# Kernel tuning notes

Measured on AMD Instinct MI355X. Metric: run time of the kernel, lower is better.

The kernel has to match this reference:

```python
import jax, jax.numpy as jnp
import numpy as np

B, N, D, H = 8, 1024, 1024, 16
P = D // H
FACTOR = 1.0 / np.sqrt(P)
DFF = 4 * D


def layernorm(x, g, b, eps=1e-5):
    mu = jnp.mean(x, axis=-1, keepdims=True)
    var = jnp.var(x, axis=-1, keepdims=True)
    return (x - mu) * jax.lax.rsqrt(var + eps) * g + b


def setup_inputs() -> dict:
    key = jax.random.key(0)
    ks = jax.random.split(key, 6)
    s = 0.02
    return {
        "x": jax.random.normal(ks[0], (B, N, D), jnp.float32),
        "prior_attn": jax.random.normal(ks[1], (B, N, N), jnp.float32),
        "Wqkv": jax.random.normal(ks[2], (D, 3 * D), jnp.float32) * s,
        "bqkv": jnp.zeros((3 * D,), jnp.float32),
        "alpha": jnp.asarray(1.0, jnp.float32),
        "ln1_g": jnp.ones((D,), jnp.float32),
        "ln1_b": jnp.zeros((D,), jnp.float32),
        "ln2_g": jnp.ones((D,), jnp.float32),
        "ln2_b": jnp.zeros((D,), jnp.float32),
        "w1": jax.random.normal(ks[3], (D, DFF), jnp.float32) * s,
        "b1": jnp.zeros((DFF,), jnp.float32),
        "w2": jax.random.normal(ks[4], (DFF, D), jnp.float32) * s,
        "b2": jnp.zeros((D,), jnp.float32),
    }


def reference(x, prior_attn, Wqkv, bqkv, alpha, ln1_g, ln1_b, ln2_g, ln2_b, w1, b1, w2, b2):
    b, n, d = x.shape
    # --- PriorMSA on ln_1(x) ---
    z1 = layernorm(x, ln1_g, ln1_b)
    qkv = z1 @ Wqkv + bqkv                      # [b, n, 3d]
    q, k, v = jnp.split(qkv, 3, axis=-1)
    q = q.reshape(b, n, H, P)
    k = k.reshape(b, n, H, P)
    v = v.reshape(b, n, H, P)
    raw = jnp.einsum('bihp,bjhp->bhij', q, k)   # [b, h, n, n]
    raw = raw + alpha * prior_attn[:, None, :, :]
    attn = jax.nn.softmax(raw * FACTOR, axis=-1)
    out = jnp.einsum('bhij,bjhp->bihp', attn, v).reshape(b, n, d)
    s1 = x + out                                 # residual (no out-projection in source)
    # --- MLP on ln_2(s1) ---
    z2 = layernorm(s1, ln2_g, ln2_b)
    mlp = jax.nn.gelu(z2 @ w1 + b1) @ w2 + b2
    return s1 + mlp
```

## Files before the change

kernel.cpp:

```cpp
#include <hip/hip_runtime.h>
#include <hip/hip_bf16.h>
#include <stdint.h>


typedef __attribute__((ext_vector_type(8))) short short8;
typedef __attribute__((ext_vector_type(4))) float f32x4;

__device__ __forceinline__ int is_bf16_in(const void* ln1g) {
  return *(const uint32_t*)ln1g == 0x3F803F80u;
}
__device__ __forceinline__ float bf2f(uint16_t u) {
  union { uint32_t i; float f; } v; v.i = ((uint32_t)u) << 16; return v.f;
}
__device__ __forceinline__ uint16_t f2bf(float f) {
  union { float f; uint32_t i; } v; v.f = f;
  uint32_t r = v.i + 0x7FFFu + ((v.i >> 16) & 1u);
  return (uint16_t)(r >> 16);
}
__device__ __forceinline__ float ldin(const void* p, size_t i, int bf) {
  return bf ? bf2f(((const uint16_t*)p)[i]) : ((const float*)p)[i];
}
__device__ __forceinline__ uint32_t pack_bf(float a, float b) {
  union { float f; uint32_t u; } ua, ub; ua.f = a; ub.f = b;
  return ((ua.u + 0x8000u) >> 16) | ((ub.u + 0x8000u) & 0xFFFF0000u);
}

typedef __attribute__((address_space(1))) void gvoid;
typedef __attribute__((address_space(3))) void lvoid;
__device__ __forceinline__ void gld16(const uint16_t* g, uint16_t* l) {
  __builtin_amdgcn_global_load_lds((const gvoid*)g, (lvoid*)l, 16, 0, 0);
}

__device__ __forceinline__ float gelu_f(float x) {
  float t1 = x * x;
  float s = fmaf(t1, -0.1029498f, -2.3023457f);
  float e = __builtin_amdgcn_exp2f(x * s);
  return x * __builtin_amdgcn_rcpf(1.0f + e);
}

template<int EPI>
__global__ __launch_bounds__(256) void gemm_bt(
    const uint16_t* __restrict__ A, const uint16_t* __restrict__ Bt,
    const void* __restrict__ bias, const void* __restrict__ flagsrc,
    void* __restrict__ Cout, const float* __restrict__ resid,
    int M, int N, int K)
{
  __shared__ __align__(16) uint16_t As[8192];
  __shared__ __align__(16) uint16_t Bs[8192];
  const int t = threadIdx.x;
  const int wv = t >> 6;
  const int lane = t & 63;
  const int ln = lane & 15, quad = lane >> 4;
  const int wm = (wv & 1) * 64, wn = (wv >> 1) * 64;
  const int row0 = blockIdx.y * 128, col0 = blockIdx.x * 128;

  auto mk = [&](const uint16_t* Pb, int base, int c) -> const uint16_t* {
    int m = c >> 3, s = c & 7;
    int kc = s ^ (m & 7);
    return Pb + (size_t)(base + m) * K + kc * 8;
  };
  const uint16_t* ap[4];
  const uint16_t* bp[4];
  uint16_t* lA[4];
  uint16_t* lB[4];
#pragma unroll
  for (int q = 0; q < 4; ++q) {
    ap[q] = mk(A, row0, t + q * 256);
    bp[q] = mk(Bt, col0, t + q * 256);
    lA[q] = &As[(q * 256 + wv * 64) * 8];
    lB[q] = &Bs[(q * 256 + wv * 64) * 8];
  }

  int aidx[2][4], bidx[2][4];
#pragma unroll
  for (int kh = 0; kh < 2; ++kh) {
#pragma unroll
    for (int i = 0; i < 4; ++i) {
      int m = wm + i * 16 + ln;
      aidx[kh][i] = (m * 8 + ((kh * 4 + quad) ^ (m & 7))) * 8;
      int n = wn + i * 16 + ln;
      bidx[kh][i] = (n * 8 + ((kh * 4 + quad) ^ (n & 7))) * 8;
    }
  }

  f32x4 acc[4][4];
#pragma unroll
  for (int i = 0; i < 4; ++i)
#pragma unroll
    for (int j = 0; j < 4; ++j) acc[i][j] = (f32x4){0.f, 0.f, 0.f, 0.f};

  for (int kt = 0; kt < K; kt += 64) {
    __syncthreads();
#pragma unroll
    for (int q = 0; q < 4; ++q) gld16(ap[q] + kt, lA[q]);
#pragma unroll
    for (int q = 0; q < 4; ++q) gld16(bp[q] + kt, lB[q]);
    __syncthreads();
#pragma unroll
    for (int kh = 0; kh < 2; ++kh) {
      short8 av[4], bv[4];
#pragma unroll
      for (int i = 0; i < 4; ++i) av[i] = *(const short8*)&As[aidx[kh][i]];
#pragma unroll
      for (int j = 0; j < 4; ++j) bv[j] = *(const short8*)&Bs[bidx[kh][j]];
#pragma unroll
      for (int i = 0; i < 4; ++i)
#pragma unroll
        for (int j = 0; j < 4; ++j)
          acc[i][j] = __builtin_amdgcn_mfma_f32_16x16x32_bf16(bv[j], av[i], acc[i][j], 0, 0, 0);
    }
  }

  const int bf = is_bf16_in(flagsrc);
#pragma unroll
  for (int j = 0; j < 4; ++j) {
    int gc0 = col0 + wn + j * 16 + quad * 4;
    float bs[4];
    if (!bf) {
      f32x4 bv4 = *(const f32x4*)((const float*)bias + gc0);
      bs[0] = bv4[0]; bs[1] = bv4[1]; bs[2] = bv4[2]; bs[3] = bv4[3];
    } else {
      ushort4 bu = *(const ushort4*)((const uint16_t*)bias + gc0);
      bs[0] = bf2f(bu.x); bs[1] = bf2f(bu.y); bs[2] = bf2f(bu.z); bs[3] = bf2f(bu.w);
    }
#pragma unroll
    for (int i = 0; i < 4; ++i) {
      int gr = row0 + wm + i * 16 + ln;
      size_t oi = (size_t)gr * N + gc0;
      float v0 = acc[i][j][0] + bs[0];
      float v1 = acc[i][j][1] + bs[1];
      float v2 = acc[i][j][2] + bs[2];
      float v3 = acc[i][j][3] + bs[3];
      if (EPI == 0) {
        uint2 pk; pk.x = pack_bf(v0, v1); pk.y = pack_bf(v2, v3);
        *(uint2*)((uint16_t*)Cout + oi) = pk;
      } else if (EPI == 1) {
        v0 = gelu_f(v0); v1 = gelu_f(v1); v2 = gelu_f(v2); v3 = gelu_f(v3);
        uint2 pk; pk.x = pack_bf(v0, v1); pk.y = pack_bf(v2, v3);
        *(uint2*)((uint16_t*)Cout + oi) = pk;
      } else {
        f32x4 rv = *(const f32x4*)(resid + oi);
        f32x4 ov = (f32x4){v0 + rv[0], v1 + rv[1], v2 + rv[2], v3 + rv[3]};
        *(f32x4*)((float*)Cout + oi) = ov;
      }
    }
  }
}

__global__ __launch_bounds__(256) void ln_rows(
    const void* __restrict__ in, int in_f32ws,
    const void* __restrict__ g_, const void* __restrict__ b_,
    uint16_t* __restrict__ out, const void* __restrict__ flagsrc)
{
  const int row = blockIdx.x;
  const int t = threadIdx.x;
  const int bf = is_bf16_in(flagsrc);
  size_t base = (size_t)row * 1024;
  float v[4];
  if (in_f32ws || !bf) {
    f32x4 vv = *(const f32x4*)((const float*)in + base + t * 4);
    v[0] = vv[0]; v[1] = vv[1]; v[2] = vv[2]; v[3] = vv[3];
  } else {
    ushort4 u = *(const ushort4*)((const uint16_t*)in + base + t * 4);
    v[0] = bf2f(u.x); v[1] = bf2f(u.y); v[2] = bf2f(u.z); v[3] = bf2f(u.w);
  }
  float s = v[0] + v[1] + v[2] + v[3];
  float q = v[0]*v[0] + v[1]*v[1] + v[2]*v[2] + v[3]*v[3];
#pragma unroll
  for (int m = 1; m < 64; m <<= 1) {
    s += __shfl_xor(s, m);
    q += __shfl_xor(q, m);
  }
  __shared__ float red[8];
  if ((t & 63) == 0) { red[t >> 6] = s; red[4 + (t >> 6)] = q; }
  __syncthreads();
  s = red[0] + red[1] + red[2] + red[3];
  q = red[4] + red[5] + red[6] + red[7];
  float mu = s * (1.0f / 1024.0f);
  float var = q * (1.0f / 1024.0f) - mu * mu;
  float rs = rsqrtf(var + 1e-5f);
  int c = t * 4;
  float gg[4], bb[4];
  if (!bf) {
    f32x4 gv = *(const f32x4*)((const float*)g_ + c);
    f32x4 bv = *(const f32x4*)((const float*)b_ + c);
    gg[0]=gv[0]; gg[1]=gv[1]; gg[2]=gv[2]; gg[3]=gv[3];
    bb[0]=bv[0]; bb[1]=bv[1]; bb[2]=bv[2]; bb[3]=bv[3];
  } else {
    ushort4 gv = *(const ushort4*)((const uint16_t*)g_ + c);
    ushort4 bv = *(const ushort4*)((const uint16_t*)b_ + c);
    gg[0]=bf2f(gv.x); gg[1]=bf2f(gv.y); gg[2]=bf2f(gv.z); gg[3]=bf2f(gv.w);
    bb[0]=bf2f(bv.x); bb[1]=bf2f(bv.y); bb[2]=bf2f(bv.z); bb[3]=bf2f(bv.w);
  }
  uint2 o;
  o.x = pack_bf((v[0] - mu) * rs * gg[0] + bb[0], (v[1] - mu) * rs * gg[1] + bb[1]);
  o.y = pack_bf((v[2] - mu) * rs * gg[2] + bb[2], (v[3] - mu) * rs * gg[3] + bb[3]);
  *(uint2*)(out + base + c) = o;
}

__global__ __launch_bounds__(256) void transpose_w(
    const void* __restrict__ W, uint16_t* __restrict__ Wt,
    int Kd, int Nw, const void* __restrict__ flagsrc)
{
  __shared__ float T[64][65];
  const int bf = is_bf16_in(flagsrc);
  int n0 = blockIdx.x * 64, k0 = blockIdx.y * 64;
  int t = threadIdx.x;
#pragma unroll
  for (int it = 0; it < 16; ++it) {
    int idx = t + it * 256;
    int r = idx >> 6, c = idx & 63;
    T[r][c] = ldin(W, (size_t)(k0 + r) * Nw + n0 + c, bf);
  }
  __syncthreads();
#pragma unroll
  for (int it = 0; it < 16; ++it) {
    int idx = t + it * 256;
    int rr = idx >> 6, cc = idx & 63;
    Wt[(size_t)(n0 + rr) * Kd + k0 + cc] = f2bf(T[cc][rr]);
  }
}

__global__ __launch_bounds__(256) void transpose_v(
    const uint16_t* __restrict__ qkv, uint16_t* __restrict__ vT)
{
  __shared__ uint16_t T[64][65];
  int n0 = blockIdx.x * 64;
  int h = blockIdx.y, b = blockIdx.z;
  int t = threadIdx.x;
#pragma unroll
  for (int it = 0; it < 16; ++it) {
    int idx = t + it * 256;
    int r = idx >> 6, c = idx & 63;
    T[r][c] = qkv[(size_t)(b * 1024 + n0 + r) * 3072 + 2048 + h * 64 + c];
  }
  __syncthreads();
#pragma unroll
  for (int it = 0; it < 16; ++it) {
    int idx = t + it * 256;
    int rr = idx >> 6, cc = idx & 63;
    vT[(size_t)((b * 16 + h) * 64 + rr) * 1024 + n0 + cc] = T[cc][rr];
  }
}

__global__ __launch_bounds__(256) void prior_cvt(
    const void* __restrict__ prior, uint16_t* __restrict__ out,
    const void* __restrict__ flagsrc)
{
  const int bf = is_bf16_in(flagsrc);
  size_t i = ((size_t)blockIdx.x * 256 + threadIdx.x) * 4;
  if (bf) {
    *(ushort4*)(out + i) = *(const ushort4*)((const uint16_t*)prior + i);
  } else {
    f32x4 v = *(const f32x4*)((const float*)prior + i);
    uint2 pk; pk.x = pack_bf(v[0], v[1]); pk.y = pack_bf(v[2], v[3]);
    *(uint2*)(out + i) = pk;
  }
}

__global__ __launch_bounds__(256) void attn_fused3(
    const uint16_t* __restrict__ qkv, const uint16_t* __restrict__ vT,
    const uint16_t* __restrict__ priorb, const void* __restrict__ x,
    const void* __restrict__ alpha_p, const void* __restrict__ flagsrc,
    float* __restrict__ s1)
{
  __shared__ __align__(16) uint16_t sm[18432];
  uint16_t* Ks = sm;
  uint16_t* Vs = sm + 4608;
  uint16_t* Ss = sm + 9216;
  float* Obuf = (float*)sm;

  const int t = threadIdx.x;
  const int w = t >> 6, lane = t & 63, ln = lane & 15, quad = lane >> 4;
  const int q0 = blockIdx.x * 128;
  const int h = blockIdx.y, b = blockIdx.z;
  const int bf = is_bf16_in(flagsrc);
  const float alpha = ldin(alpha_p, 0, bf);
  const float c1 = 0.125f * 1.44269504088896340736f;
  const float c2 = alpha * c1;
  uint16_t* Ssw = Ss + w * 2304;

  const int r8 = t >> 3, c8 = t & 7;

  short8 qf[2][2];
#pragma unroll
  for (int qt = 0; qt < 2; ++qt) {
    const uint16_t* qsrc = &qkv[(size_t)(b * 1024 + q0 + 32 * w + 16 * qt + ln) * 3072 + h * 64 + quad * 8];
    qf[qt][0] = *(const short8*)qsrc;
    qf[qt][1] = *(const short8*)(qsrc + 32);
  }

  const uint16_t* kbase = &qkv[(size_t)(b * 1024 + r8) * 3072 + 1024 + h * 64 + c8 * 8];
  const uint16_t* vbase = &vT[(size_t)((b * 16 + h) * 64 + r8) * 1024 + c8 * 8];
  uint4 kr0 = *(const uint4*)kbase;
  uint4 kr1 = *(const uint4*)(kbase + (size_t)32 * 3072);
  uint4 vr0 = *(const uint4*)vbase;
  uint4 vr1 = *(const uint4*)(vbase + (size_t)32 * 1024);

  f32x4 o[4][2];
#pragma unroll
  for (int i = 0; i < 4; ++i) { o[i][0] = (f32x4){0.f,0.f,0.f,0.f}; o[i][1] = (f32x4){0.f,0.f,0.f,0.f}; }
  float accl[2] = {0.f, 0.f};

  for (int j = 0; j < 16; ++j) {
    __syncthreads();
    *(uint4*)&Ks[r8 * 72 + c8 * 8] = kr0;
    *(uint4*)&Ks[(r8 + 32) * 72 + c8 * 8] = kr1;
    *(uint4*)&Vs[r8 * 72 + c8 * 8] = vr0;
    *(uint4*)&Vs[(r8 + 32) * 72 + c8 * 8] = vr1;
    __syncthreads();
    if (j < 15) {
      const uint16_t* kp = kbase + (size_t)(j + 1) * 64 * 3072;
      kr0 = *(const uint4*)kp;
      kr1 = *(const uint4*)(kp + (size_t)32 * 3072);
      const uint16_t* vp = vbase + (j + 1) * 64;
      vr0 = *(const uint4*)vp;
      vr1 = *(const uint4*)(vp + (size_t)32 * 1024);
    }
    ushort4 pv[2][4];
#pragma unroll
    for (int qt = 0; qt < 2; ++qt) {
      const uint16_t* pb = priorb + ((size_t)(b * 1024 + q0 + 32 * w + 16 * qt + ln)) * 1024 + j * 64 + 4 * quad;
#pragma unroll
      for (int nt = 0; nt < 4; ++nt) pv[qt][nt] = *(const ushort4*)(pb + 16 * nt);
    }
#pragma unroll
    for (int nt = 0; nt < 4; ++nt) {
      short8 kf0 = *(const short8*)&Ks[(16 * nt + ln) * 72 + quad * 8];
      short8 kf1 = *(const short8*)&Ks[(16 * nt + ln) * 72 + 32 + quad * 8];
#pragma unroll
      for (int qt = 0; qt < 2; ++qt) {
        f32x4 z = (f32x4){0.f, 0.f, 0.f, 0.f};
        z = __builtin_amdgcn_mfma_f32_16x16x32_bf16(kf0, qf[qt][0], z, 0, 0, 0);
        z = __builtin_amdgcn_mfma_f32_16x16x32_bf16(kf1, qf[qt][1], z, 0, 0, 0);
        float p0 = __builtin_amdgcn_exp2f(z[0] * c1 + bf2f(pv[qt][nt].x) * c2);
        float p1 = __builtin_amdgcn_exp2f(z[1] * c1 + bf2f(pv[qt][nt].y) * c2);
        float p2 = __builtin_amdgcn_exp2f(z[2] * c1 + bf2f(pv[qt][nt].z) * c2);
        float p3 = __builtin_amdgcn_exp2f(z[3] * c1 + bf2f(pv[qt][nt].w) * c2);
        accl[qt] += (p0 + p1) + (p2 + p3);
        uint2 pk; pk.x = pack_bf(p0, p1); pk.y = pack_bf(p2, p3);
        *(uint2*)&Ssw[(16 * qt + ln) * 72 + 16 * nt + 4 * quad] = pk;
      }
    }
    asm volatile("" ::: "memory");
    short8 pf[2][2];
#pragma unroll
    for (int qt = 0; qt < 2; ++qt) {
      pf[qt][0] = *(const short8*)&Ssw[(16 * qt + ln) * 72 + quad * 8];
      pf[qt][1] = *(const short8*)&Ssw[(16 * qt + ln) * 72 + 32 + quad * 8];
    }
#pragma unroll
    for (int dt = 0; dt < 4; ++dt) {
      short8 vf0 = *(const short8*)&Vs[(16 * dt + ln) * 72 + quad * 8];
      short8 vf1 = *(const short8*)&Vs[(16 * dt + ln) * 72 + 32 + quad * 8];
#pragma unroll
      for (int qt = 0; qt < 2; ++qt) {
        o[dt][qt] = __builtin_amdgcn_mfma_f32_16x16x32_bf16(vf0, pf[qt][0], o[dt][qt], 0, 0, 0);
        o[dt][qt] = __builtin_amdgcn_mfma_f32_16x16x32_bf16(vf1, pf[qt][1], o[dt][qt], 0, 0, 0);
      }
    }
  }

  float inv[2];
#pragma unroll
  for (int qt = 0; qt < 2; ++qt) {
    float a = accl[qt];
    a += __shfl_xor(a, 16);
    a += __shfl_xor(a, 32);
    inv[qt] = 1.0f / a;
  }

  __syncthreads();
#pragma unroll
  for (int qt = 0; qt < 2; ++qt)
#pragma unroll
    for (int dt = 0; dt < 4; ++dt) {
      f32x4 ov = o[dt][qt] * inv[qt];
      *(f32x4*)&Obuf[(32 * w + 16 * qt + ln) * 68 + 16 * dt + 4 * quad] = ov;
    }
  __syncthreads();
#pragma unroll
  for (int half = 0; half < 2; ++half) {
    int row = half * 64 + (t >> 2), cc0 = (t & 3) * 16;
    size_t gbase = ((size_t)(b * 1024 + q0 + row)) * 1024 + h * 64 + cc0;
#pragma unroll
    for (int i = 0; i < 4; ++i) {
      f32x4 ov = *(const f32x4*)&Obuf[row * 68 + cc0 + 4 * i];
      f32x4 xr;
      if (!bf) {
        xr = *(const f32x4*)((const float*)x + gbase + 4 * i);
      } else {
        ushort4 xu = *(const ushort4*)((const uint16_t*)x + gbase + 4 * i);
        xr = (f32x4){bf2f(xu.x), bf2f(xu.y), bf2f(xu.z), bf2f(xu.w)};
      }
      *(f32x4*)(s1 + gbase + 4 * i) = ov + xr;
    }
  }
}

extern "C" void kernel_launch(void* const* d_in, const int* in_sizes, int n_in,
                              void* d_out, int out_size, void* d_ws, size_t ws_size,
                              hipStream_t stream)
{
  const void* x     = d_in[0];
  const void* prior = d_in[1];
  const void* Wqkv  = d_in[2];
  const void* bqkv  = d_in[3];
  const void* alpha = d_in[4];
  const void* ln1g  = d_in[5];
  const void* ln1b  = d_in[6];
  const void* ln2g  = d_in[7];
  const void* ln2b  = d_in[8];
  const void* w1    = d_in[9];
  const void* b1    = d_in[10];
  const void* w2    = d_in[11];
  const void* b2    = d_in[12];

  char* ws = (char*)d_ws;
  uint16_t* wqkvt = (uint16_t*)(ws + 256);
  uint16_t* w1t   = (uint16_t*)(ws + 6291712);
  uint16_t* w2t   = (uint16_t*)(ws + 14680320);
  uint16_t* z     = (uint16_t*)(ws + 23068928);
  uint16_t* qkv   = (uint16_t*)(ws + 39846144);
  uint16_t* vT    = (uint16_t*)(ws + 90177792);
  float*    s1    = (float*)(ws + 106955008);
  uint16_t* h1    = qkv;
  uint16_t* priorb = z;

  transpose_w<<<dim3(48, 16), 256, 0, stream>>>(Wqkv, wqkvt, 1024, 3072, ln1g);
  transpose_w<<<dim3(64, 16), 256, 0, stream>>>(w1, w1t, 1024, 4096, ln1g);
  transpose_w<<<dim3(16, 64), 256, 0, stream>>>(w2, w2t, 4096, 1024, ln1g);
  ln_rows<<<8192, 256, 0, stream>>>(x, 0, ln1g, ln1b, z, ln1g);
  gemm_bt<0><<<dim3(24, 64), 256, 0, stream>>>(z, wqkvt, bqkv, ln1g, qkv, nullptr, 8192, 3072, 1024);
  prior_cvt<<<8192, 256, 0, stream>>>(prior, priorb, ln1g);
  transpose_v<<<dim3(16, 16, 8), 256, 0, stream>>>(qkv, vT);
  attn_fused3<<<dim3(8, 16, 8), 256, 0, stream>>>(qkv, vT, priorb, x, alpha, ln1g, s1);
  ln_rows<<<8192, 256, 0, stream>>>(s1, 1, ln2g, ln2b, z, ln1g);
  gemm_bt<1><<<dim3(32, 64), 256, 0, stream>>>(z, w1t, b1, ln1g, h1, nullptr, 8192, 4096, 1024);
  gemm_bt<2><<<dim3(8, 64), 256, 0, stream>>>(h1, w2t, b2, ln1g, d_out, s1, 8192, 1024, 4096);
}
```

Baseline: 579.1 us.

## Load K/V MFMA fragments directly from global, drop LDS staging and block syncs

The attention kernel no longer stages K and V tiles through shared memory with two barriers per iteration. Each wave now loads its MFMA fragments straight from global memory (relying on L2/L1 reuse across waves) and writes the output directly without an LDS transpose. Alpha times the scale is folded into the prior during the bf16 conversion, so the inner loop uses a single fma. It also adds a perm-based bf16 pack and a launch bound of four blocks per SM. The cost is redundant global/L1 traffic, since the four waves of a block now each fetch the same K/V, and the folded prior is rounded to bf16 after scaling.

```diff
diff --git a/kernel.cpp b/kernel.cpp
--- a/kernel.cpp
+++ b/kernel.cpp
@@ -23,6 +23,10 @@
 __device__ __forceinline__ uint32_t pack_bf(float a, float b) {
   union { float f; uint32_t u; } ua, ub; ua.f = a; ub.f = b;
   return ((ua.u + 0x8000u) >> 16) | ((ub.u + 0x8000u) & 0xFFFF0000u);
+}
+__device__ __forceinline__ uint32_t pack_bf_perm(float a, float b) {
+  union { float f; uint32_t u; } ua, ub; ua.f = a; ub.f = b;
+  return __builtin_amdgcn_perm(ub.u + 0x8000u, ua.u + 0x8000u, 0x03020706u);
 }
 
 typedef __attribute__((address_space(1))) void gvoid;
@@ -245,42 +249,38 @@
 
 __global__ __launch_bounds__(256) void prior_cvt(
     const void* __restrict__ prior, uint16_t* __restrict__ out,
-    const void* __restrict__ flagsrc)
+    const void* __restrict__ alpha_p, const void* __restrict__ flagsrc)
 {
   const int bf = is_bf16_in(flagsrc);
+  const float c = ldin(alpha_p, 0, bf) * 0.125f * 1.44269504088896340736f;
   size_t i = ((size_t)blockIdx.x * 256 + threadIdx.x) * 4;
+  float v0, v1, v2, v3;
   if (bf) {
-    *(ushort4*)(out + i) = *(const ushort4*)((const uint16_t*)prior + i);
+    ushort4 u = *(const ushort4*)((const uint16_t*)prior + i);
+    v0 = bf2f(u.x); v1 = bf2f(u.y); v2 = bf2f(u.z); v3 = bf2f(u.w);
   } else {
     f32x4 v = *(const f32x4*)((const float*)prior + i);
-    uint2 pk; pk.x = pack_bf(v[0], v[1]); pk.y = pack_bf(v[2], v[3]);
-    *(uint2*)(out + i) = pk;
-  }
-}
-
-__global__ __launch_bounds__(256) void attn_fused3(
+    v0 = v[0]; v1 = v[1]; v2 = v[2]; v3 = v[3];
+  }
+  uint2 pk;
+  pk.x = pack_bf(v0 * c, v1 * c);
+  pk.y = pack_bf(v2 * c, v3 * c);
+  *(uint2*)(out + i) = pk;
+}
+
+__global__ __launch_bounds__(256, 4) void attn_fused4(
     const uint16_t* __restrict__ qkv, const uint16_t* __restrict__ vT,
     const uint16_t* __restrict__ priorb, const void* __restrict__ x,
-    const void* __restrict__ alpha_p, const void* __restrict__ flagsrc,
-    float* __restrict__ s1)
-{
-  __shared__ __align__(16) uint16_t sm[18432];
-  uint16_t* Ks = sm;
-  uint16_t* Vs = sm + 4608;
-  uint16_t* Ss = sm + 9216;
-  float* Obuf = (float*)sm;
-
+    const void* __restrict__ flagsrc, float* __restrict__ s1)
+{
+  __shared__ __align__(16) uint16_t Ss[4 * 2304];
   const int t = threadIdx.x;
   const int w = t >> 6, lane = t & 63, ln = lane & 15, quad = lane >> 4;
   const int q0 = blockIdx.x * 128;
   const int h = blockIdx.y, b = blockIdx.z;
   const int bf = is_bf16_in(flagsrc);
-  const float alpha = ldin(alpha_p, 0, bf);
   const float c1 = 0.125f * 1.44269504088896340736f;
-  const float c2 = alpha * c1;
   uint16_t* Ssw = Ss + w * 2304;
-
-  const int r8 = t >> 3, c8 = t & 7;
 
   short8 qf[2][2];
 #pragma unroll
@@ -290,12 +290,9 @@
     qf[qt][1] = *(const short8*)(qsrc + 32);
   }
 
-  const uint16_t* kbase = &qkv[(size_t)(b * 1024 + r8) * 3072 + 1024 + h * 64 + c8 * 8];
-  const uint16_t* vbase = &vT[(size_t)((b * 16 + h) * 64 + r8) * 1024 + c8 * 8];
-  uint4 kr0 = *(const uint4*)kbase;
-  uint4 kr1 = *(const uint4*)(kbase + (size_t)32 * 3072);
-  uint4 vr0 = *(const uint4*)vbase;
-  uint4 vr1 = *(const uint4*)(vbase + (size_t)32 * 1024);
+  const uint16_t* kb = qkv + (size_t)(b * 1024 + 16 * 0 + ln) * 3072 + 1024 + h * 64 + quad * 8;
+  const uint16_t* vb = vT + (size_t)((b * 16 + h) * 64 + ln) * 1024 + quad * 8;
+  const uint16_t* prb = priorb + (size_t)(b * 1024 + q0 + 32 * w + ln) * 1024 + 4 * quad;
 
   f32x4 o[4][2];
 #pragma unroll
@@ -303,42 +300,35 @@
   float accl[2] = {0.f, 0.f};
 
   for (int j = 0; j < 16; ++j) {
-    __syncthreads();
-    *(uint4*)&Ks[r8 * 72 + c8 * 8] = kr0;
-    *(uint4*)&Ks[(r8 + 32) * 72 + c8 * 8] = kr1;
-    *(uint4*)&Vs[r8 * 72 + c8 * 8] = vr0;
-    *(uint4*)&Vs[(r8 + 32) * 72 + c8 * 8] = vr1;
-    __syncthreads();
-    if (j < 15) {
-      const uint16_t* kp = kbase + (size_t)(j + 1) * 64 * 3072;
-      kr0 = *(const uint4*)kp;
-      kr1 = *(const uint4*)(kp + (size_t)32 * 3072);
-      const uint16_t* vp = vbase + (j + 1) * 64;
-      vr0 = *(const uint4*)vp;
-      vr1 = *(const uint4*)(vp + (size_t)32 * 1024);
+    short8 kf[4][2];
+#pragma unroll
+    for (int nt = 0; nt < 4; ++nt) {
+      const uint16_t* kp = kb + (size_t)(j * 64 + 16 * nt) * 3072;
+      kf[nt][0] = *(const short8*)kp;
+      kf[nt][1] = *(const short8*)(kp + 32);
     }
     ushort4 pv[2][4];
 #pragma unroll
     for (int qt = 0; qt < 2; ++qt) {
-      const uint16_t* pb = priorb + ((size_t)(b * 1024 + q0 + 32 * w + 16 * qt + ln)) * 1024 + j * 64 + 4 * quad;
-#pragma unroll
-      for (int nt = 0; nt < 4; ++nt) pv[qt][nt] = *(const ushort4*)(pb + 16 * nt);
+      const uint16_t* pp = prb + (size_t)(16 * qt) * 1024 + j * 64;
+#pragma unroll
+      for (int nt = 0; nt < 4; ++nt) pv[qt][nt] = *(const ushort4*)(pp + 16 * nt);
     }
 #pragma unroll
     for (int nt = 0; nt < 4; ++nt) {
-      short8 kf0 = *(const short8*)&Ks[(16 * nt + ln) * 72 + quad * 8];
-      short8 kf1 = *(const short8*)&Ks[(16 * nt + ln) * 72 + 32 + quad * 8];
 #pragma unroll
       for (int qt = 0; qt < 2; ++qt) {
         f32x4 z = (f32x4){0.f, 0.f, 0.f, 0.f};
-        z = __builtin_amdgcn_mfma_f32_16x16x32_bf16(kf0, qf[qt][0], z, 0, 0, 0);
-        z = __builtin_amdgcn_mfma_f32_16x16x32_bf16(kf1, qf[qt][1], z, 0, 0, 0);
-        float p0 = __builtin_amdgcn_exp2f(z[0] * c1 + bf2f(pv[qt][nt].x) * c2);
-        float p1 = __builtin_amdgcn_exp2f(z[1] * c1 + bf2f(pv[qt][nt].y) * c2);
-        float p2 = __builtin_amdgcn_exp2f(z[2] * c1 + bf2f(pv[qt][nt].z) * c2);
-        float p3 = __builtin_amdgcn_exp2f(z[3] * c1 + bf2f(pv[qt][nt].w) * c2);
+        z = __builtin_amdgcn_mfma_f32_16x16x32_bf16(kf[nt][0], qf[qt][0], z, 0, 0, 0);
+        z = __builtin_amdgcn_mfma_f32_16x16x32_bf16(kf[nt][1], qf[qt][1], z, 0, 0, 0);
+        float p0 = __builtin_amdgcn_exp2f(fmaf(z[0], c1, bf2f(pv[qt][nt].x)));
+        float p1 = __builtin_amdgcn_exp2f(fmaf(z[1], c1, bf2f(pv[qt][nt].y)));
+        float p2 = __builtin_amdgcn_exp2f(fmaf(z[2], c1, bf2f(pv[qt][nt].z)));
+        float p3 = __builtin_amdgcn_exp2f(fmaf(z[3], c1, bf2f(pv[qt][nt].w)));
         accl[qt] += (p0 + p1) + (p2 + p3);
-        uint2 pk; pk.x = pack_bf(p0, p1); pk.y = pack_bf(p2, p3);
+        uint2 pk;
+        pk.x = pack_bf_perm(p0, p1);
+        pk.y = pack_bf_perm(p2, p3);
         *(uint2*)&Ssw[(16 * qt + ln) * 72 + 16 * nt + 4 * quad] = pk;
       }
     }
@@ -351,8 +341,9 @@
     }
 #pragma unroll
     for (int dt = 0; dt < 4; ++dt) {
-      short8 vf0 = *(const short8*)&Vs[(16 * dt + ln) * 72 + quad * 8];
-      short8 vf1 = *(const short8*)&Vs[(16 * dt + ln) * 72 + 32 + quad * 8];
+      const uint16_t* vp = vb + (size_t)(16 * dt) * 1024 + j * 64;
+      short8 vf0 = *(const short8*)vp;
+      short8 vf1 = *(const short8*)(vp + 32);
 #pragma unroll
       for (int qt = 0; qt < 2; ++qt) {
         o[dt][qt] = __builtin_amdgcn_mfma_f32_16x16x32_bf16(vf0, pf[qt][0], o[dt][qt], 0, 0, 0);
@@ -370,30 +361,21 @@
     inv[qt] = 1.0f / a;
   }
 
-  __syncthreads();
-#pragma unroll
-  for (int qt = 0; qt < 2; ++qt)
+#pragma unroll
+  for (int qt = 0; qt < 2; ++qt) {
+    size_t rbase = ((size_t)(b * 1024 + q0 + 32 * w + 16 * qt + ln)) * 1024 + h * 64 + 4 * quad;
 #pragma unroll
     for (int dt = 0; dt < 4; ++dt) {
-      f32x4 ov = o[dt][qt] * inv[qt];
-      *(f32x4*)&Obuf[(32 * w + 16 * qt + ln) * 68 + 16 * dt + 4 * quad] = ov;
-    }
-  __syncthreads();
-#pragma unroll
-  for (int half = 0; half < 2; ++half) {
-    int row = half * 64 + (t >> 2), cc0 = (t & 3) * 16;
-    size_t gbase = ((size_t)(b * 1024 + q0 + row)) * 1024 + h * 64 + cc0;
-#pragma unroll
-    for (int i = 0; i < 4; ++i) {
-      f32x4 ov = *(const f32x4*)&Obuf[row * 68 + cc0 + 4 * i];
+      size_t oi = rbase + 16 * dt;
       f32x4 xr;
       if (!bf) {
-        xr = *(const f32x4*)((const float*)x + gbase + 4 * i);
+        xr = *(const f32x4*)((const float*)x + oi);
       } else {
-        ushort4 xu = *(const ushort4*)((const uint16_t*)x + gbase + 4 * i);
+        ushort4 xu = *(const ushort4*)((const uint16_t*)x + oi);
         xr = (f32x4){bf2f(xu.x), bf2f(xu.y), bf2f(xu.z), bf2f(xu.w)};
       }
-      *(f32x4*)(s1 + gbase + 4 * i) = ov + xr;
+      f32x4 ov = o[dt][qt] * inv[qt] + xr;
+      *(f32x4*)(s1 + oi) = ov;
     }
   }
 }
@@ -432,9 +414,9 @@
   transpose_w<<<dim3(16, 64), 256, 0, stream>>>(w2, w2t, 4096, 1024, ln1g);
   ln_rows<<<8192, 256, 0, stream>>>(x, 0, ln1g, ln1b, z, ln1g);
   gemm_bt<0><<<dim3(24, 64), 256, 0, stream>>>(z, wqkvt, bqkv, ln1g, qkv, nullptr, 8192, 3072, 1024);
-  prior_cvt<<<8192, 256, 0, stream>>>(prior, priorb, ln1g);
+  prior_cvt<<<8192, 256, 0, stream>>>(prior, priorb, alpha, ln1g);
   transpose_v<<<dim3(16, 16, 8), 256, 0, stream>>>(qkv, vT);
-  attn_fused3<<<dim3(8, 16, 8), 256, 0, stream>>>(qkv, vT, priorb, x, alpha, ln1g, s1);
+  attn_fused4<<<dim3(8, 16, 8), 256, 0, stream>>>(qkv, vT, priorb, x, ln1g, s1);
   ln_rows<<<8192, 256, 0, stream>>>(s1, 1, ln2g, ln2b, z, ln1g);
   gemm_bt<1><<<dim3(32, 64), 256, 0, stream>>>(z, w1t, b1, ln1g, h1, nullptr, 8192, 4096, 1024);
   gemm_bt<2><<<dim3(8, 64), 256, 0, stream>>>(h1, w2t, b2, ln1g, d_out, s1, 8192, 1024, 4096);
```

Result: slower. 645.9 us (+11.5%).
